# Optimization experiments

Hardware: AMD Instinct MI355X
Metric: run time of the kernel (lower is better)

Reference implementation:

```python
import jax, jax.numpy as jnp
import numpy as np

B, C, H, W = 16, 256, 56, 56
NH = 8           # num_heads
BS = 8           # block_size
HALO = 3         # halo_size
WIN = BS + 2 * HALO   # 14
MLP = 4


def setup_inputs() -> dict:
    key = jax.random.key(0)
    ks = jax.random.split(key, 8)
    f = lambda k, shape, s: jax.random.normal(k, shape, jnp.float32) * s
    return dict(
        x=jax.random.normal(ks[0], (B, C, H, W), jnp.float32),
        ln1_g=jnp.ones((C,), jnp.float32), ln1_b=jnp.zeros((C,), jnp.float32),
        wq=f(ks[1], (C, C), C ** -0.5), bq=jnp.zeros((C,), jnp.float32),
        wkv=f(ks[2], (2 * C, C), C ** -0.5), bkv=jnp.zeros((2 * C,), jnp.float32),
        bias=f(ks[3], (1, NH, 1, BS * BS, WIN * WIN), 0.02),
        gamma1=jnp.full((1, C, 1, 1), 1e-6, jnp.float32),
        ln2_g=jnp.ones((C,), jnp.float32), ln2_b=jnp.zeros((C,), jnp.float32),
        w1=f(ks[4], (MLP * C, C), 0.02), b1=jnp.zeros((MLP * C,), jnp.float32),
        w2=f(ks[5], (C, MLP * C), 0.02), b2=jnp.zeros((C,), jnp.float32),
        gamma2=jnp.full((1, 1, 1, C), 1e-6, jnp.float32),
    )


def _ln2d(x, g, b, eps=1e-5):
    # LayerNorm over channel dim of NCHW
    mu = jnp.mean(x, axis=1, keepdims=True)
    var = jnp.mean((x - mu) ** 2, axis=1, keepdims=True)
    return (x - mu) * jax.lax.rsqrt(var + eps) * g[None, :, None, None] + b[None, :, None, None]


def _halo_attn(x, wq, bq, wkv, bkv, bias):
    Bn, Cc, Hh, Ww = x.shape
    dh = Cc // NH
    scale = dh ** -0.5
    nHb, nWb = Hh // BS, Ww // BS
    xh = jnp.transpose(x, (0, 2, 3, 1))            # B,H,W,C
    q = xh @ wq.T + bq                             # 1x1 conv
    kv = xh @ wkv.T + bkv                          # B,H,W,2C
    # q blocks: B,nh,nblocks,bs^2,dh
    q = q.reshape(Bn, nHb, BS, nWb, BS, NH, dh).transpose(0, 5, 1, 3, 2, 4, 6)
    q = q.reshape(Bn, NH, nHb * nWb, BS * BS, dh)
    # kv halo windows
    kvp = jnp.pad(kv, ((0, 0), (HALO, HALO), (HALO, HALO), (0, 0)))
    ih = (jnp.arange(nHb) * BS)[:, None] + jnp.arange(WIN)[None, :]
    iw = (jnp.arange(nWb) * BS)[:, None] + jnp.arange(WIN)[None, :]
    kvw = kvp[:, ih[:, None, :, None], iw[None, :, None, :], :]
    kvw = kvw.reshape(Bn, nHb * nWb, WIN * WIN, NH, 2 * dh).transpose(0, 3, 1, 2, 4)
    k, v = kvw[..., :dh], kvw[..., dh:]
    attn = jnp.einsum('bhnqd,bhnkd->bhnqk', q, k) * scale + bias
    attn = jax.nn.softmax(attn, axis=-1)
    out = jnp.einsum('bhnqk,bhnkd->bhnqd', attn, v)                   # B,nh,nb,bs^2,dh
    out = out.reshape(Bn, NH, nHb, nWb, BS, BS, dh).transpose(0, 1, 6, 2, 4, 3, 5)
    return out.reshape(Bn, Cc, Hh, Ww)


def _forward(x, ln1_g, ln1_b, wq, bq, wkv, bkv, bias, gamma1,
             ln2_g, ln2_b, w1, b1, w2, b2, gamma2):
    shortcut = x
    a = _halo_attn(_ln2d(x, ln1_g, ln1_b), wq, bq, wkv, bkv, bias)
    x = shortcut + gamma1 * a
    shortcut = x
    y = jnp.transpose(_ln2d(x, ln2_g, ln2_b), (0, 2, 3, 1))           # NHWC
    y = jax.nn.gelu(y @ w1.T + b1, approximate=False) @ w2.T + b2
    y = gamma2 * y
    return shortcut + jnp.transpose(y, (0, 3, 1, 2))


def reference(x, ln1_g, ln1_b, wq, bq, wkv, bkv, bias, gamma1,
              ln2_g, ln2_b, w1, b1, w2, b2, gamma2):
    return _forward(x, ln1_g, ln1_b, wq, bq, wkv, bkv, bias, gamma1,
                    ln2_g, ln2_b, w1, b1, w2, b2, gamma2)
```

## Files before the change

### kernel.cpp

```cpp
#include <hip/hip_runtime.h>
#include <hip/hip_bf16.h>
#include <math.h>

typedef unsigned short u16;
typedef float f32x4 __attribute__((ext_vector_type(4)));
typedef __bf16 bf16x8 __attribute__((ext_vector_type(8)));

__device__ __forceinline__ float bf2f(u16 u) {
    union { float f; unsigned int i; } v; v.i = ((unsigned int)u) << 16; return v.f;
}
__device__ __forceinline__ u16 f2bf(float f) {
    union { float f; unsigned int i; } v; v.f = f;
    unsigned int x = v.i;
    return (u16)((x + 0x7FFFu + ((x >> 16) & 1u)) >> 16);
}

__global__ __launch_bounds__(256) void k_prep(const float* __restrict__ wq, const float* __restrict__ wkv,
                                              const float* __restrict__ w1, const float* __restrict__ w2,
                                              u16* __restrict__ wqkvb, u16* __restrict__ w1p, u16* __restrict__ w2p) {
    const int bid = blockIdx.x, t = threadIdx.x;
    if (bid < 192) {
        int e = (bid * 256 + t) * 4;
        const float* src = (e < 65536) ? (wq + e) : (wkv + (e - 65536));
        float4 v = *(const float4*)src;
        ushort4 o;
        o.x = f2bf(v.x); o.y = f2bf(v.y); o.z = f2bf(v.z); o.w = f2bf(v.w);
        *(ushort4*)(wqkvb + e) = o;
    } else if (bid < 320) {
        int tid = (bid - 192) * 256 + t;
        int kc = tid >> 11, rem = tid & 2047;
        int wave = rem >> 9, rem2 = rem & 511;
        int ks = rem2 >> 6, lane = rem2 & 63;
        int ln = lane & 15, quad = lane >> 4;
        const float* src = w1 + (size_t)(kc * 64 + wave * 16 + ln) * 256 + ks * 32 + quad * 8;
        float4 v0 = *(const float4*)src;
        float4 v1 = *(const float4*)(src + 4);
        alignas(16) u16 tmp[8];
        tmp[0] = f2bf(v0.x); tmp[1] = f2bf(v0.y); tmp[2] = f2bf(v0.z); tmp[3] = f2bf(v0.w);
        tmp[4] = f2bf(v1.x); tmp[5] = f2bf(v1.y); tmp[6] = f2bf(v1.z); tmp[7] = f2bf(v1.w);
        *(int4*)(w1p + (size_t)tid * 8) = *(int4*)tmp;
    } else {
        int tid = (bid - 320) * 256 + t;
        int kc = tid >> 11, rem = tid & 2047;
        int wave = rem >> 9, rem2 = rem & 511;
        int ks2 = rem2 >> 8, rem3 = rem2 & 255;
        int nt = rem3 >> 6, lane = rem3 & 63;
        int ln = lane & 15, quad = lane >> 4;
        const float* src = w2 + (size_t)(wave * 64 + nt * 16 + ln) * 1024 + kc * 64 + ks2 * 32 + quad * 8;
        float4 v0 = *(const float4*)src;
        float4 v1 = *(const float4*)(src + 4);
        alignas(16) u16 tmp[8];
        tmp[0] = f2bf(v0.x); tmp[1] = f2bf(v0.y); tmp[2] = f2bf(v0.z); tmp[3] = f2bf(v0.w);
        tmp[4] = f2bf(v1.x); tmp[5] = f2bf(v1.y); tmp[6] = f2bf(v1.z); tmp[7] = f2bf(v1.w);
        *(int4*)(w2p + (size_t)tid * 8) = *(int4*)tmp;
    }
}

__global__ __launch_bounds__(256) void k_transpose(const float* __restrict__ x, u16* __restrict__ xh) {
    __shared__ __align__(16) u16 tile[64][72];
    const int t = threadIdx.x;
    const int hw0 = blockIdx.x * 64;
    const int c0  = blockIdx.y * 64;
    const int b   = blockIdx.z;
    const int cl = t >> 2, wl = (t & 3) * 16;
    {
        int c = c0 + cl;
        const float* src = x + (size_t)(b * 256 + c) * 3136 + hw0 + wl;
        for (int q = 0; q < 4; q++) {
            float4 v = *(const float4*)(src + q * 4);
            u16* dst = &tile[cl][wl + q * 4];
            dst[0] = f2bf(v.x); dst[1] = f2bf(v.y); dst[2] = f2bf(v.z); dst[3] = f2bf(v.w);
        }
    }
    __syncthreads();
    const int hl = t >> 3, cl2 = (t & 7) * 8;
    for (int i = 0; i < 2; i++) {
        int hw = hl + i * 32;
        alignas(16) u16 tmp[8];
        for (int j = 0; j < 8; j++) tmp[j] = tile[cl2 + j][hw];
        u16* dst = xh + (size_t)(b * 3136 + hw0 + hw) * 256 + c0 + cl2;
        *(int4*)dst = *(int4*)tmp;
    }
}

__global__ __launch_bounds__(256) void k_ln(const u16* __restrict__ in, u16* __restrict__ out,
                                            const float* __restrict__ g, const float* __restrict__ bta) {
    const int wave = threadIdx.x >> 6, lane = threadIdx.x & 63;
    const int p = blockIdx.x * 4 + wave;
    ushort4 v = *(const ushort4*)(in + (size_t)p * 256 + lane * 4);
    float f0 = bf2f(v.x), f1 = bf2f(v.y), f2 = bf2f(v.z), f3 = bf2f(v.w);
    float s = f0 + f1 + f2 + f3;
    float sq = f0 * f0 + f1 * f1 + f2 * f2 + f3 * f3;
    for (int o = 32; o >= 1; o >>= 1) { s += __shfl_xor(s, o, 64); sq += __shfl_xor(sq, o, 64); }
    float m = s * (1.f / 256.f);
    float var = sq * (1.f / 256.f) - m * m;
    float inv = rsqrtf(var + 1e-5f);
    float4 gv = *(const float4*)(g + lane * 4);
    float4 bv = *(const float4*)(bta + lane * 4);
    ushort4 o4;
    o4.x = f2bf((f0 - m) * inv * gv.x + bv.x);
    o4.y = f2bf((f1 - m) * inv * gv.y + bv.y);
    o4.z = f2bf((f2 - m) * inv * gv.z + bv.z);
    o4.w = f2bf((f3 - m) * inv * gv.w + bv.w);
    *(ushort4*)(out + (size_t)p * 256 + lane * 4) = o4;
}

__global__ __launch_bounds__(256) void k_qkv(
    const u16* __restrict__ xn, const u16* __restrict__ Bw,
    const float* __restrict__ bq, const float* __restrict__ bkv,
    u16* __restrict__ out) {
    __shared__ __align__(16) u16 smem[17408];
    u16* As = smem;
    u16* Bs = smem + 4096;

    const int g = blockIdx.x;
    const int xcd = g & 7, idx = g >> 3;
    const int bm = xcd * 49 + idx / 6, bn = idx % 6;

    const int t = threadIdx.x;
    const int wave = t >> 6, lane = t & 63;
    const int wm = (wave >> 1) * 64, wn = (wave & 1) * 64;
    const int ln = lane & 15, quad = lane >> 4;

    f32x4 vzero = {0.f, 0.f, 0.f, 0.f};
    f32x4 acc[4][4];
    for (int i = 0; i < 4; i++) for (int j = 0; j < 4; j++) acc[i][j] = vzero;

    const int srow = t >> 2;
    const int scol = (t & 3) * 8;

    for (int k0 = 0; k0 < 256; k0 += 32) {
        for (int i = 0; i < 2; i++) {
            int r = srow + i * 64;
            *(int4*)&As[r * 32 + scol] = *(const int4*)(xn + (size_t)(bm * 128 + r) * 256 + k0 + scol);
            *(int4*)&Bs[r * 32 + scol] = *(const int4*)(Bw + (size_t)(bn * 128 + r) * 256 + k0 + scol);
        }
        __syncthreads();
        bf16x8 af[4], bfr[4];
        for (int mt = 0; mt < 4; mt++) af[mt] = *(const bf16x8*)&As[(wm + mt * 16 + ln) * 32 + quad * 8];
        for (int nt = 0; nt < 4; nt++) bfr[nt] = *(const bf16x8*)&Bs[(wn + nt * 16 + ln) * 32 + quad * 8];
        for (int mt = 0; mt < 4; mt++)
            for (int nt = 0; nt < 4; nt++)
                acc[mt][nt] = __builtin_amdgcn_mfma_f32_16x16x32_bf16(bfr[nt], af[mt], acc[mt][nt], 0, 0, 0);
        __syncthreads();
    }

    u16* Cs = smem;
    for (int nt = 0; nt < 4; nt++) {
        int gn0 = bn * 128 + wn + nt * 16 + quad * 4;
        f32x4 bv = (gn0 < 256) ? *(const f32x4*)(bq + gn0) : *(const f32x4*)(bkv + gn0 - 256);
        for (int mt = 0; mt < 4; mt++) {
            ushort4 pk;
            pk.x = f2bf(acc[mt][nt][0] + bv[0]);
            pk.y = f2bf(acc[mt][nt][1] + bv[1]);
            pk.z = f2bf(acc[mt][nt][2] + bv[2]);
            pk.w = f2bf(acc[mt][nt][3] + bv[3]);
            *(ushort4*)&Cs[(wm + mt * 16 + ln) * 136 + wn + nt * 16 + quad * 4] = pk;
        }
    }
    __syncthreads();
    const int row = t >> 4, col = (t & 15) * 8;
    for (int pass = 0; pass < 8; pass++) {
        int rr = pass * 16 + row;
        int4 v = *(int4*)&Cs[rr * 136 + col];
        *(int4*)(out + (size_t)(bm * 128 + rr) * 768 + bn * 128 + col) = v;
    }
}

__global__ __launch_bounds__(256) void k_mlp(
    const u16* __restrict__ xn, const u16* __restrict__ x2,
    const u16* __restrict__ w1p, const float* __restrict__ b1,
    const u16* __restrict__ w2p, const float* __restrict__ b2,
    const float* __restrict__ g2v, float* __restrict__ outT) {
    __shared__ __align__(16) u16 smem[16896 + 2 * 8704];
    u16* As = smem;

    const int g = blockIdx.x;
    const int bm = (g & 7) * 98 + (g >> 3);

    const int t = threadIdx.x;
    const int wave = t >> 6, lane = t & 63;
    const int ln = lane & 15, quad = lane >> 4;
    const int wn64 = wave * 64;
    const int wq4 = (wave >> 1) * 4 + (wave & 1) * 2;

    f32x4 vzero = {0.f, 0.f, 0.f, 0.f};
    f32x4 acc[4][4];
    for (int i = 0; i < 4; i++) for (int j = 0; j < 4; j++) acc[i][j] = vzero;

    {
        const int srow = t >> 2, scb = (t & 3) * 8;
        for (int c = 0; c < 8; c++) {
            int col = scb + c * 32;
            *(int4*)&As[srow * 264 + col] = *(const int4*)(xn + (size_t)(bm * 64 + srow) * 256 + col);
        }
    }
    __syncthreads();

    for (int kc = 0; kc < 8; kc++) {
        u16* Hs = smem + 16896 + (kc & 1) * 8704;
        bf16x8 w1f[2][8];
        {
            const u16* w1b = w1p + (size_t)(kc * 8 + wq4) * 4096 + lane * 8;
            #pragma unroll
            for (int nt = 0; nt < 2; nt++)
                #pragma unroll
                for (int ks = 0; ks < 8; ks++)
                    w1f[nt][ks] = *(const bf16x8*)(w1b + nt * 4096 + ks * 512);
        }
        f32x4 up[4][2];
        #pragma unroll
        for (int i = 0; i < 4; i++) { up[i][0] = vzero; up[i][1] = vzero; }
        #pragma unroll
        for (int ks = 0; ks < 8; ks++) {
            #pragma unroll
            for (int mt = 0; mt < 4; mt++) {
                bf16x8 af = *(const bf16x8*)&As[(mt * 16 + ln) * 264 + ks * 32 + quad * 8];
                up[mt][0] = __builtin_amdgcn_mfma_f32_16x16x32_bf16(w1f[0][ks], af, up[mt][0], 0, 0, 0);
                up[mt][1] = __builtin_amdgcn_mfma_f32_16x16x32_bf16(w1f[1][ks], af, up[mt][1], 0, 0, 0);
            }
        }
        bf16x8 w2f[4][4];
        #pragma unroll
        for (int ks2 = 0; ks2 < 4; ks2++) {
            const u16* w2b = w2p + (size_t)((((kc * 2 + (ks2 >> 1)) * 4 + wave) * 2 + (ks2 & 1)) * 4) * 512 + lane * 8;
            #pragma unroll
            for (int nt = 0; nt < 4; nt++)
                w2f[ks2][nt] = *(const bf16x8*)(w2b + nt * 512);
        }
        #pragma unroll
        for (int nt = 0; nt < 2; nt++) {
            float4 bv = *(const float4*)(b1 + kc * 128 + wave * 32 + nt * 16 + quad * 4);
            #pragma unroll
            for (int mt = 0; mt < 4; mt++) {
                float v0 = up[mt][nt][0] + bv.x;
                float v1 = up[mt][nt][1] + bv.y;
                float v2 = up[mt][nt][2] + bv.z;
                float v3 = up[mt][nt][3] + bv.w;
                ushort4 pk;
                pk.x = f2bf(v0 * (1.f / (1.f + __expf(-1.702f * v0))));
                pk.y = f2bf(v1 * (1.f / (1.f + __expf(-1.702f * v1))));
                pk.z = f2bf(v2 * (1.f / (1.f + __expf(-1.702f * v2))));
                pk.w = f2bf(v3 * (1.f / (1.f + __expf(-1.702f * v3))));
                *(ushort4*)&Hs[(mt * 16 + ln) * 136 + wave * 32 + nt * 16 + quad * 4] = pk;
            }
        }
        __syncthreads();
        #pragma unroll
        for (int ks2 = 0; ks2 < 4; ks2++) {
            bf16x8 hf[4];
            #pragma unroll
            for (int mt = 0; mt < 4; mt++)
                hf[mt] = *(const bf16x8*)&Hs[(mt * 16 + ln) * 136 + ks2 * 32 + quad * 8];
            #pragma unroll
            for (int nt = 0; nt < 4; nt++) {
                #pragma unroll
                for (int mt = 0; mt < 4; mt++)
                    acc[mt][nt] = __builtin_amdgcn_mfma_f32_16x16x32_bf16(hf[mt], w2f[ks2][nt], acc[mt][nt], 0, 0, 0);
            }
        }
    }

    const int b = bm / 49;
    for (int nt = 0; nt < 4; nt++) {
        int gn = wn64 + nt * 16 + ln;
        float bs = b2[gn], g2 = g2v[gn];
        for (int mt = 0; mt < 4; mt++) {
            int gm0 = bm * 64 + mt * 16 + quad * 4;
            int hw0 = gm0 - b * 3136;
            f32x4 res;
            for (int r = 0; r < 4; r++)
                res[r] = bf2f(x2[(size_t)(gm0 + r) * 256 + gn]) + g2 * (acc[mt][nt][r] + bs);
            *(f32x4*)(outT + (size_t)(b * 256 + gn) * 3136 + hw0) = res;
        }
    }
}

__global__ __launch_bounds__(256) void k_attn(
    const u16* __restrict__ qkv, const float* __restrict__ bias,
    const u16* __restrict__ xh, const float* __restrict__ gamma1,
    u16* __restrict__ x2) {
    __shared__ __align__(16) u16 Kl[208 * 40];
    __shared__ __align__(16) u16 Vt[32 * 232];
    __shared__ __align__(16) u16 Pl[4][16 * 232];

    const int t = threadIdx.x;
    const int blk = blockIdx.x, head = blockIdx.y, b = blockIdx.z;
    const int bh = blk / 7, bw = blk - bh * 7;
    const int wave = t >> 6, lane = t & 63;
    const int ln = lane & 15, quad = lane >> 4;

    {
        int4 z = {0, 0, 0, 0};
        for (int i = t; i < (32 * 232) / 8; i += 256) ((int4*)Vt)[i] = z;
        for (int i = t; i < (4 * 16 * 232) / 8; i += 256) ((int4*)&Pl[0][0])[i] = z;
    }
    __syncthreads();

    for (int cid = t; cid < 208 * 8; cid += 256) {
        int pos = cid >> 3, part = cid & 7;
        int i = pos / 14, j = pos - i * 14;
        int gh = bh * 8 - 3 + i, gw = bw * 8 - 3 + j;
        bool valid = (pos < 196) && ((unsigned)gh < 56u) && ((unsigned)gw < 56u);
        int d0 = (part & 3) * 8;
        int4 v = {0, 0, 0, 0};
        if (valid) {
            size_t p = (size_t)(b * 56 + gh) * 56 + gw;
            v = *(const int4*)(qkv + p * 768 + 256 + head * 64 + ((part & 4) ? 32 : 0) + d0);
        }
        if (!(part & 4)) {
            *(int4*)&Kl[pos * 40 + d0] = v;
        } else {
            alignas(16) u16 tmp[8];
            *(int4*)tmp = v;
            for (int jj = 0; jj < 8; jj++) Vt[(d0 + jj) * 232 + pos] = tmp[jj];
        }
    }
    __syncthreads();

    const int qrow = wave * 16 + ln;
    const int qh = bh * 8 + (qrow >> 3), qw = bw * 8 + (qrow & 7);
    const size_t qp = (size_t)(b * 56 + qh) * 56 + qw;
    bf16x8 qf = *(const bf16x8*)(qkv + qp * 768 + head * 32 + quad * 8);

    f32x4 vzero = {0.f, 0.f, 0.f, 0.f};
    float sv[13][4];
    float mx[4] = {-1e30f, -1e30f, -1e30f, -1e30f};
    const float scale = 0.17677669529663687f;
    for (int nt = 0; nt < 13; nt++) {
        bf16x8 kf = *(const bf16x8*)&Kl[(nt * 16 + ln) * 40 + quad * 8];
        f32x4 s = __builtin_amdgcn_mfma_f32_16x16x32_bf16(qf, kf, vzero, 0, 0, 0);
        int kk = nt * 16 + ln;
        bool kvalid = kk < 196;
        for (int r = 0; r < 4; r++) {
            int qq = wave * 16 + quad * 4 + r;
            float val = kvalid ? (s[r] * scale + bias[(size_t)(head * 64 + qq) * 196 + kk]) : -1e30f;
            sv[nt][r] = val;
            mx[r] = fmaxf(mx[r], val);
        }
    }
    for (int o = 1; o < 16; o <<= 1)
        for (int r = 0; r < 4; r++) mx[r] = fmaxf(mx[r], __shfl_xor(mx[r], o, 16));
    float sum[4] = {0.f, 0.f, 0.f, 0.f};
    for (int nt = 0; nt < 13; nt++)
        for (int r = 0; r < 4; r++) {
            float e = __expf(sv[nt][r] - mx[r]);
            sv[nt][r] = e;
            sum[r] += e;
        }
    for (int o = 1; o < 16; o <<= 1)
        for (int r = 0; r < 4; r++) sum[r] += __shfl_xor(sum[r], o, 16);
    float rinv[4];
    for (int r = 0; r < 4; r++) rinv[r] = 1.f / sum[r];

    u16* plw = &Pl[wave][0];
    for (int nt = 0; nt < 13; nt++)
        for (int r = 0; r < 4; r++)
            plw[(quad * 4 + r) * 232 + nt * 16 + ln] = f2bf(sv[nt][r]);
    __syncthreads();

    f32x4 o_acc[2];
    o_acc[0] = vzero; o_acc[1] = vzero;
    for (int kc = 0; kc < 7; kc++) {
        bf16x8 pf = *(const bf16x8*)&plw[ln * 232 + kc * 32 + quad * 8];
        for (int n2 = 0; n2 < 2; n2++) {
            bf16x8 vf = *(const bf16x8*)&Vt[(n2 * 16 + ln) * 232 + kc * 32 + quad * 8];
            o_acc[n2] = __builtin_amdgcn_mfma_f32_16x16x32_bf16(pf, vf, o_acc[n2], 0, 0, 0);
        }
    }

    for (int n2 = 0; n2 < 2; n2++) {
        int c = head * 32 + n2 * 16 + ln;
        float g1 = gamma1[c];
        for (int r = 0; r < 4; r++) {
            int q = wave * 16 + quad * 4 + r;
            int hh = bh * 8 + (q >> 3), ww = bw * 8 + (q & 7);
            size_t p = (size_t)(b * 56 + hh) * 56 + ww;
            float a = o_acc[n2][r] * rinv[r];
            x2[p * 256 + c] = f2bf(bf2f(xh[p * 256 + c]) + g1 * a);
        }
    }
}

extern "C" void kernel_launch(void* const* d_in, const int* in_sizes, int n_in,
                              void* d_out, int out_size, void* d_ws, size_t ws_size,
                              hipStream_t stream) {
    const float* x      = (const float*)d_in[0];
    const float* ln1_g  = (const float*)d_in[1];
    const float* ln1_b  = (const float*)d_in[2];
    const float* wq     = (const float*)d_in[3];
    const float* bq     = (const float*)d_in[4];
    const float* wkv    = (const float*)d_in[5];
    const float* bkv    = (const float*)d_in[6];
    const float* bias   = (const float*)d_in[7];
    const float* gamma1 = (const float*)d_in[8];
    const float* ln2_g  = (const float*)d_in[9];
    const float* ln2_b  = (const float*)d_in[10];
    const float* w1     = (const float*)d_in[11];
    const float* b1     = (const float*)d_in[12];
    const float* w2     = (const float*)d_in[13];
    const float* b2     = (const float*)d_in[14];
    const float* gamma2 = (const float*)d_in[15];

    char* ws = (char*)d_ws;
    u16* qkv   = (u16*)ws;
    u16* xh    = (u16*)(ws + 77070336);
    u16* x2    = (u16*)(ws + 102760448);
    u16* wqkvb = (u16*)(ws + 128450560);
    u16* w1p   = (u16*)(ws + 128843776);
    u16* w2p   = (u16*)(ws + 129368064);
    u16* xn1   = x2;
    u16* xn2   = xh;

    k_prep<<<dim3(448), 256, 0, stream>>>(wq, wkv, w1, w2, wqkvb, w1p, w2p);
    k_transpose<<<dim3(49, 4, 16), 256, 0, stream>>>(x, xh);
    k_ln<<<dim3(12544), 256, 0, stream>>>(xh, xn1, ln1_g, ln1_b);
    k_qkv<<<dim3(2352), 256, 0, stream>>>(xn1, wqkvb, bq, bkv, qkv);
    k_attn<<<dim3(49, 8, 16), 256, 0, stream>>>(qkv, bias, xh, gamma1, x2);
    k_ln<<<dim3(12544), 256, 0, stream>>>(x2, xn2, ln2_g, ln2_b);
    k_mlp<<<dim3(784), 256, 0, stream>>>(xn2, x2, w1p, b1, w2p, b2, gamma2, (float*)d_out);
}
```

Baseline: 393.1 us.

## Keep attention probabilities in registers and fold scale and bias into MFMA

```diff
diff --git a/kernel.cpp b/kernel.cpp
--- a/kernel.cpp
+++ b/kernel.cpp
@@ -13,6 +13,11 @@
     union { float f; unsigned int i; } v; v.f = f;
     unsigned int x = v.i;
     return (u16)((x + 0x7FFFu + ((x >> 16) & 1u)) >> 16);
+}
+__device__ __forceinline__ unsigned int cvt_pk_bf16(float lo, float hi) {
+    unsigned int r;
+    asm("v_cvt_pk_bf16_f32 %0, %1, %2" : "=v"(r) : "v"(lo), "v"(hi));
+    return r;
 }
 
 __global__ __launch_bounds__(256) void k_prep(const float* __restrict__ wq, const float* __restrict__ wkv,
@@ -22,9 +27,10 @@
     if (bid < 192) {
         int e = (bid * 256 + t) * 4;
         const float* src = (e < 65536) ? (wq + e) : (wkv + (e - 65536));
+        float sc = (e < 65536) ? 0.17677669529663687f : 1.f;
         float4 v = *(const float4*)src;
         ushort4 o;
-        o.x = f2bf(v.x); o.y = f2bf(v.y); o.z = f2bf(v.z); o.w = f2bf(v.w);
+        o.x = f2bf(v.x * sc); o.y = f2bf(v.y * sc); o.z = f2bf(v.z * sc); o.w = f2bf(v.w * sc);
         *(ushort4*)(wqkvb + e) = o;
     } else if (bid < 320) {
         int tid = (bid - 192) * 256 + t;
@@ -148,7 +154,13 @@
     u16* Cs = smem;
     for (int nt = 0; nt < 4; nt++) {
         int gn0 = bn * 128 + wn + nt * 16 + quad * 4;
-        f32x4 bv = (gn0 < 256) ? *(const f32x4*)(bq + gn0) : *(const f32x4*)(bkv + gn0 - 256);
+        f32x4 bv;
+        if (gn0 < 256) {
+            f32x4 tq = *(const f32x4*)(bq + gn0);
+            bv = tq * 0.17677669529663687f;
+        } else {
+            bv = *(const f32x4*)(bkv + gn0 - 256);
+        }
         for (int mt = 0; mt < 4; mt++) {
             ushort4 pk;
             pk.x = f2bf(acc[mt][nt][0] + bv[0]);
@@ -276,26 +288,18 @@
     }
 }
 
-__global__ __launch_bounds__(256) void k_attn(
+__global__ __launch_bounds__(256, 4) void k_attn(
     const u16* __restrict__ qkv, const float* __restrict__ bias,
     const u16* __restrict__ xh, const float* __restrict__ gamma1,
     u16* __restrict__ x2) {
     __shared__ __align__(16) u16 Kl[208 * 40];
-    __shared__ __align__(16) u16 Vt[32 * 232];
-    __shared__ __align__(16) u16 Pl[4][16 * 232];
+    __shared__ __align__(16) u16 Vt[32 * 236];
 
     const int t = threadIdx.x;
     const int blk = blockIdx.x, head = blockIdx.y, b = blockIdx.z;
     const int bh = blk / 7, bw = blk - bh * 7;
     const int wave = t >> 6, lane = t & 63;
     const int ln = lane & 15, quad = lane >> 4;
-
-    {
-        int4 z = {0, 0, 0, 0};
-        for (int i = t; i < (32 * 232) / 8; i += 256) ((int4*)Vt)[i] = z;
-        for (int i = t; i < (4 * 16 * 232) / 8; i += 256) ((int4*)&Pl[0][0])[i] = z;
-    }
-    __syncthreads();
 
     for (int cid = t; cid < 208 * 8; cid += 256) {
         int pos = cid >> 3, part = cid & 7;
@@ -313,7 +317,7 @@
         } else {
             alignas(16) u16 tmp[8];
             *(int4*)tmp = v;
-            for (int jj = 0; jj < 8; jj++) Vt[(d0 + jj) * 232 + pos] = tmp[jj];
+            for (int jj = 0; jj < 8; jj++) Vt[(d0 + jj) * 236 + pos] = tmp[jj];
         }
     }
     __syncthreads();
@@ -323,60 +327,85 @@
     const size_t qp = (size_t)(b * 56 + qh) * 56 + qw;
     bf16x8 qf = *(const bf16x8*)(qkv + qp * 768 + head * 32 + quad * 8);
 
-    f32x4 vzero = {0.f, 0.f, 0.f, 0.f};
-    float sv[13][4];
-    float mx[4] = {-1e30f, -1e30f, -1e30f, -1e30f};
-    const float scale = 0.17677669529663687f;
+    f32x4 s[13];
+    const float* bp = bias + (size_t)(head * 64 + qrow) * 196 + quad * 4;
+    #pragma unroll
     for (int nt = 0; nt < 13; nt++) {
         bf16x8 kf = *(const bf16x8*)&Kl[(nt * 16 + ln) * 40 + quad * 8];
-        f32x4 s = __builtin_amdgcn_mfma_f32_16x16x32_bf16(qf, kf, vzero, 0, 0, 0);
-        int kk = nt * 16 + ln;
-        bool kvalid = kk < 196;
+        f32x4 c;
+        if (nt < 12 || quad == 0) {
+            c = *(const f32x4*)(bp + nt * 16);
+        } else {
+            c = (f32x4){-1e30f, -1e30f, -1e30f, -1e30f};
+        }
+        s[nt] = __builtin_amdgcn_mfma_f32_16x16x32_bf16(kf, qf, c, 0, 0, 0);
+    }
+
+    float mx = -1e30f;
+    #pragma unroll
+    for (int nt = 0; nt < 13; nt++)
+        #pragma unroll
+        for (int r = 0; r < 4; r++) mx = fmaxf(mx, s[nt][r]);
+    mx = fmaxf(mx, __shfl_xor(mx, 16, 64));
+    mx = fmaxf(mx, __shfl_xor(mx, 32, 64));
+    float sum = 0.f;
+    #pragma unroll
+    for (int nt = 0; nt < 13; nt++)
+        #pragma unroll
         for (int r = 0; r < 4; r++) {
-            int qq = wave * 16 + quad * 4 + r;
-            float val = kvalid ? (s[r] * scale + bias[(size_t)(head * 64 + qq) * 196 + kk]) : -1e30f;
-            sv[nt][r] = val;
-            mx[r] = fmaxf(mx[r], val);
-        }
-    }
-    for (int o = 1; o < 16; o <<= 1)
-        for (int r = 0; r < 4; r++) mx[r] = fmaxf(mx[r], __shfl_xor(mx[r], o, 16));
-    float sum[4] = {0.f, 0.f, 0.f, 0.f};
-    for (int nt = 0; nt < 13; nt++)
-        for (int r = 0; r < 4; r++) {
-            float e = __expf(sv[nt][r] - mx[r]);
-            sv[nt][r] = e;
-            sum[r] += e;
-        }
-    for (int o = 1; o < 16; o <<= 1)
-        for (int r = 0; r < 4; r++) sum[r] += __shfl_xor(sum[r], o, 16);
-    float rinv[4];
-    for (int r = 0; r < 4; r++) rinv[r] = 1.f / sum[r];
-
-    u16* plw = &Pl[wave][0];
-    for (int nt = 0; nt < 13; nt++)
-        for (int r = 0; r < 4; r++)
-            plw[(quad * 4 + r) * 232 + nt * 16 + ln] = f2bf(sv[nt][r]);
-    __syncthreads();
-
+            float e = __expf(s[nt][r] - mx);
+            s[nt][r] = e;
+            sum += e;
+        }
+    sum += __shfl_xor(sum, 16, 64);
+    sum += __shfl_xor(sum, 32, 64);
+    float rinv = 1.f / sum;
+
+    unsigned int pk[13][2];
+    #pragma unroll
+    for (int nt = 0; nt < 13; nt++) {
+        pk[nt][0] = cvt_pk_bf16(s[nt][0], s[nt][1]);
+        pk[nt][1] = cvt_pk_bf16(s[nt][2], s[nt][3]);
+    }
+
+    f32x4 vzero = {0.f, 0.f, 0.f, 0.f};
     f32x4 o_acc[2];
     o_acc[0] = vzero; o_acc[1] = vzero;
+    #pragma unroll
     for (int kc = 0; kc < 7; kc++) {
-        bf16x8 pf = *(const bf16x8*)&plw[ln * 232 + kc * 32 + quad * 8];
+        union { int4 i4; bf16x8 v; } pu;
+        pu.i4.x = pk[2 * kc][0];
+        pu.i4.y = pk[2 * kc][1];
+        pu.i4.z = (kc < 6) ? pk[2 * kc + 1][0] : 0;
+        pu.i4.w = (kc < 6) ? pk[2 * kc + 1][1] : 0;
+        #pragma unroll
         for (int n2 = 0; n2 < 2; n2++) {
-            bf16x8 vf = *(const bf16x8*)&Vt[(n2 * 16 + ln) * 232 + kc * 32 + quad * 8];
-            o_acc[n2] = __builtin_amdgcn_mfma_f32_16x16x32_bf16(pf, vf, o_acc[n2], 0, 0, 0);
-        }
-    }
-
+            union { int4 i4; bf16x8 v; } vu;
+            const u16* vb = &Vt[(n2 * 16 + ln) * 236 + kc * 32 + quad * 4];
+            *(int2*)&vu.i4.x = *(const int2*)vb;
+            if (kc < 6) {
+                *(int2*)&vu.i4.z = *(const int2*)(vb + 16);
+            } else {
+                vu.i4.z = 0; vu.i4.w = 0;
+            }
+            o_acc[n2] = __builtin_amdgcn_mfma_f32_16x16x32_bf16(pu.v, vu.v, o_acc[n2], 0, 0, 0);
+        }
+    }
+
+    float rr4[4];
+    #pragma unroll
+    for (int r = 0; r < 4; r++) rr4[r] = __shfl(rinv, quad * 4 + r, 16);
+
+    #pragma unroll
     for (int n2 = 0; n2 < 2; n2++) {
         int c = head * 32 + n2 * 16 + ln;
         float g1 = gamma1[c];
+        #pragma unroll
         for (int r = 0; r < 4; r++) {
             int q = wave * 16 + quad * 4 + r;
             int hh = bh * 8 + (q >> 3), ww = bw * 8 + (q & 7);
             size_t p = (size_t)(b * 56 + hh) * 56 + ww;
-            float a = o_acc[n2][r] * rinv[r];
+            float a = o_acc[n2][r] * rr4[r];
             x2[p * 256 + c] = f2bf(bf2f(xh[p * 256 + c]) + g1 * a);
         }
     }
```

Result: faster. 335.4 us (-14.7%).
